# Optimization experiments

Hardware: AMD Instinct MI355X
Metric: run time of the kernel (lower is better)

The kernel has to match this reference:

```python
import jax, jax.numpy as jnp
import numpy as np

N = 50000
NEG_SLOPE = 0.2

def gat_conv(x, src, dst, W, a_src, a_dst, bias, heads, out_ch):
    # Linear projection per head: [N, H, C]
    h = (x @ W).reshape(x.shape[0], heads, out_ch)
    # Node-level attention terms alpha_src/alpha_dst: [N, H]
    al_src = jnp.einsum('nhc,hc->nh', h, a_src)
    al_dst = jnp.einsum('nhc,hc->nh', h, a_dst)
    # Edge logits with LeakyReLU: [E, H]
    logits = jax.nn.leaky_relu(al_src[src] + al_dst[dst], NEG_SLOPE)
    # Segment softmax over incoming edges of each dst node
    m = jax.ops.segment_max(logits, dst, num_segments=N)
    e = jnp.exp(logits - m[dst])
    s = jax.ops.segment_sum(e, dst, num_segments=N)
    alpha = e / (s[dst] + 1e-16)                      # [E, H]
    # Weighted message aggregation (scatter-add): [N, H, C]
    out = jax.ops.segment_sum(h[src] * alpha[..., None], dst, num_segments=N)
    return out.reshape(N, heads * out_ch) + bias


def setup_inputs() -> dict:
    key = jax.random.key(0)
    ks = jax.random.split(key, 12)
    in_ch, out_ch = 128, 256
    h1, c1 = 4, out_ch // 8          # conv1: 4 heads x 32
    mid = h1 * c1                    # 128 = out_ch // 2
    E = 1600000
    x = jax.random.normal(ks[0], (N, in_ch), jnp.float32)
    edge_index = jax.random.randint(ks[1], (2, E), 0, N, jnp.int64)
    sc = 0.1
    return {
        'x': x,
        'edge_index': edge_index,
        'W1': jax.random.normal(ks[2], (in_ch, h1 * c1), jnp.float32) * sc,
        'a_src1': jax.random.normal(ks[3], (h1, c1), jnp.float32) * sc,
        'a_dst1': jax.random.normal(ks[4], (h1, c1), jnp.float32) * sc,
        'b1': jnp.zeros((h1 * c1,), jnp.float32),
        'W2': jax.random.normal(ks[5], (mid, out_ch), jnp.float32) * sc,
        'a_src2': jax.random.normal(ks[6], (1, out_ch), jnp.float32) * sc,
        'a_dst2': jax.random.normal(ks[7], (1, out_ch), jnp.float32) * sc,
        'b2': jnp.zeros((out_ch,), jnp.float32),
    }


def reference(x, edge_index, W1, a_src1, a_dst1, b1, W2, a_src2, a_dst2, b2):
    # PyG GATConv adds self-loops by default
    loop = jnp.arange(N, dtype=edge_index.dtype)
    src = jnp.concatenate([edge_index[0], loop])
    dst = jnp.concatenate([edge_index[1], loop])
    h = gat_conv(x, src, dst, W1, a_src1, a_dst1, b1, heads=4, out_ch=32)
    h = jax.nn.relu(h)
    out = gat_conv(h, src, dst, W2, a_src2, a_dst2, b2, heads=1, out_ch=256)
    return out
```

## Files before the change

### kernel.cpp

```cpp
#include <hip/hip_runtime.h>
#include <hip/hip_fp16.h>
#include <math.h>

#define NSLOPE 0.2f

typedef _Float16 half8 __attribute__((ext_vector_type(8)));
typedef float floatx4 __attribute__((ext_vector_type(4)));

__device__ __forceinline__ float lrelu(float t) { return t > 0.f ? t : NSLOPE * t; }

__device__ __forceinline__ void fma8h(float* acc, float w, const uint4& v) {
    const __half2* h2 = reinterpret_cast<const __half2*>(&v);
#pragma unroll
    for (int i = 0; i < 4; ++i) {
        float2 f = __half22float2(h2[i]);
        acc[2 * i]     = fmaf(w, f.x, acc[2 * i]);
        acc[2 * i + 1] = fmaf(w, f.y, acc[2 * i + 1]);
    }
}

#define MAXB 5632
#define BE   8192

__global__ __launch_bounds__(256)
void prep_kernel(const int* __restrict__ dst, int* __restrict__ bcnt,
                 const float* __restrict__ x, __half* __restrict__ x16, int nx,
                 const float* __restrict__ W1, __half* __restrict__ W1T,
                 const float* __restrict__ W2, __half* __restrict__ W2T,
                 const float* __restrict__ a_src2, const float* __restrict__ a_dst2,
                 float* __restrict__ w2s, float* __restrict__ w2d,
                 int E, int Etot, int nb, int nbA, int ncast, int nt1, int nt2)
{
    __shared__ int hist[512];
    int bid = blockIdx.x;
    int tid = threadIdx.x;

    if (bid < nbA) {
        for (int i = tid; i < 512; i += 256) hist[i] = 0;
        __syncthreads();
        for (int e = bid * 256 + tid; e < Etot; e += nbA * 256) {
            int d = (e < E) ? dst[e] : (e - E);
            atomicAdd(&hist[d >> 7], 1);
        }
        __syncthreads();
        for (int i = tid; i < nb; i += 256) {
            int v = hist[i];
            if (v) atomicAdd(&bcnt[i], v);
        }
        return;
    }
    bid -= nbA;
    if (bid < ncast) {
        int i = (bid * 256 + tid) * 4;
        if (i < nx) {
            float4 v = *(const float4*)&x[i];
            __half2 a = __floats2half2_rn(v.x, v.y);
            __half2 b = __floats2half2_rn(v.z, v.w);
            *(uint2*)&x16[i] = make_uint2(*(unsigned*)&a, *(unsigned*)&b);
        }
        return;
    }
    bid -= ncast;
    if (bid < nt1) {
        int idx = bid * 256 + tid;
        int c = idx >> 7, k = idx & 127;
        W1T[(size_t)c * 128 + k] = __float2half(W1[(size_t)k * 128 + c]);
        return;
    }
    bid -= nt1;
    if (bid < nt2) {
        int idx = bid * 256 + tid;
        int c = idx >> 7, k = idx & 127;
        W2T[(size_t)c * 128 + k] = __float2half(W2[(size_t)k * 256 + c]);
        return;
    }
    {
        const float* a = (tid < 128) ? a_src2 : a_dst2;
        int k = tid & 127;
        float acc = 0.f;
        for (int c = 0; c < 256; c += 4) {
            float4 w = *(const float4*)&W2[(size_t)k * 256 + c];
            float4 av = *(const float4*)&a[c];
            acc = fmaf(w.x, av.x, fmaf(w.y, av.y, fmaf(w.z, av.z, fmaf(w.w, av.w, acc))));
        }
        if (tid < 128) w2s[k] = acc; else w2d[k] = acc;
    }
}

__global__ __launch_bounds__(512)
void scanBuckets_kernel(const int* __restrict__ bcnt, int* __restrict__ bbase,
                        int* __restrict__ gcur, int nb, int* __restrict__ offs,
                        int N, int total)
{
    __shared__ int tmp[512];
    int tid = threadIdx.x;
    int v = (tid < nb) ? bcnt[tid] : 0;
    tmp[tid] = v;
    __syncthreads();
    for (int off = 1; off < 512; off <<= 1) {
        int t = (tid >= off) ? tmp[tid - off] : 0;
        __syncthreads();
        tmp[tid] += t;
        __syncthreads();
    }
    if (tid < nb) {
        int e = tmp[tid] - v;
        bbase[tid] = e;
        gcur[tid] = e;
    }
    if (tid == 0) offs[N] = total;
}

__global__ __launch_bounds__(256)
void bucketB_kernel(const int* __restrict__ src, const int* __restrict__ dst,
                    int* __restrict__ gcur, unsigned* __restrict__ eout,
                    int E, int Etot, int nb)
{
    __shared__ int hist[512];
    __shared__ int res[512];
    __shared__ int lcur[512];
    int tid = threadIdx.x;
    int e0 = blockIdx.x * BE;
    int e1 = min(e0 + BE, Etot);

    for (int i = tid; i < 512; i += 256) hist[i] = 0;
    __syncthreads();
    for (int e = e0 + tid; e < e1; e += 256) {
        int d = (e < E) ? dst[e] : (e - E);
        atomicAdd(&hist[d >> 7], 1);
    }
    __syncthreads();
    for (int i = tid; i < nb; i += 256) {
        int h = hist[i];
        res[i] = h ? atomicAdd(&gcur[i], h) : 0;
        lcur[i] = 0;
    }
    __syncthreads();
    for (int e = e0 + tid; e < e1; e += 256) {
        int s, d;
        if (e < E) { s = src[e]; d = dst[e]; }
        else       { s = e - E; d = s; }
        int b = d >> 7;
        int p = res[b] + atomicAdd(&lcur[b], 1);
        eout[p] = (unsigned)s | ((unsigned)(d & 127) << 16);
    }
}

__global__ __launch_bounds__(256)
void combo_kernel(const unsigned* __restrict__ eout, const int* __restrict__ bbase,
                  const int* __restrict__ bcnt, unsigned short* __restrict__ csr,
                  int* __restrict__ offs, int N, int nb,
                  const __half* __restrict__ A16, const __half* __restrict__ W1T,
                  const float* __restrict__ a_src, const float* __restrict__ a_dst,
                  __half* __restrict__ h1, float* __restrict__ al_src,
                  float* __restrict__ al_dst)
{
    __shared__ unsigned eb[MAXB];
    __shared__ unsigned short sbuf[MAXB];
    __shared__ int cnt128[128], cur128[128], sc[128];

    int tid = threadIdx.x;
    if ((int)blockIdx.x < nb) {
        int b = blockIdx.x;
        int ebase = bbase[b];
        int ecnt = bcnt[b];
        int n0 = b << 7;
        int ncount = min(128, N - n0);

        if (tid < 128) cnt128[tid] = 0;
        for (int i = tid; i < ecnt; i += 256) eb[i] = eout[ebase + i];
        __syncthreads();
        for (int i = tid; i < ecnt; i += 256) atomicAdd(&cnt128[eb[i] >> 16], 1);
        __syncthreads();
        if (tid < 128) sc[tid] = cnt128[tid];
        __syncthreads();
        for (int off = 1; off < 128; off <<= 1) {
            int t = (tid >= off && tid < 128) ? sc[tid - off] : 0;
            __syncthreads();
            if (tid < 128) sc[tid] += t;
            __syncthreads();
        }
        if (tid < 128) {
            int excl = sc[tid] - cnt128[tid];
            cur128[tid] = excl;
            if (tid < ncount) offs[n0 + tid] = ebase + excl;
        }
        __syncthreads();
        for (int i = tid; i < ecnt; i += 256) {
            unsigned v = eb[i];
            int p = atomicAdd(&cur128[v >> 16], 1);
            sbuf[p] = (unsigned short)(v & 0xFFFFu);
        }
        __syncthreads();
        for (int i = tid; i < ecnt; i += 256) csr[ebase + i] = sbuf[i];
        return;
    }

    int gb = blockIdx.x - nb;
    int M = N;
    int wave = tid >> 6, lane = tid & 63;
    int lr = lane & 15, q = lane >> 4;
    int r0 = gb * 32 + (wave >> 1) * 16;
    int wcol = (wave & 1) * 64;

    int arow = min(r0 + lr, M - 1);
    const uint4* Arow = (const uint4*)A16 + (size_t)arow * 16;
    half8 a[4];
#pragma unroll
    for (int kb = 0; kb < 4; ++kb) {
        union { uint4 u; half8 h; } c;
        c.u = Arow[kb * 4 + q];
        a[kb] = c.h;
    }

    floatx4 acc[4];
    const floatx4 zero = {0.f, 0.f, 0.f, 0.f};
#pragma unroll
    for (int ct = 0; ct < 4; ++ct) acc[ct] = zero;

#pragma unroll
    for (int ct = 0; ct < 4; ++ct) {
        const uint4* Brow = (const uint4*)W1T + (size_t)(wcol + ct * 16 + lr) * 16;
#pragma unroll
        for (int kb = 0; kb < 4; ++kb) {
            union { uint4 u; half8 h; } c;
            c.u = Brow[kb * 4 + q];
            acc[ct] = __builtin_amdgcn_mfma_f32_16x16x32_f16(a[kb], c.h, acc[ct], 0, 0, 0);
        }
    }

#pragma unroll
    for (int ct = 0; ct < 4; ++ct) {
        int col = wcol + ct * 16 + lr;
#pragma unroll
        for (int r = 0; r < 4; ++r) {
            int row = r0 + q * 4 + r;
            if (row < M) h1[(size_t)row * 128 + col] = __float2half(acc[ct][r]);
        }
    }

    float as[4], ad[4];
#pragma unroll
    for (int ct = 0; ct < 4; ++ct) {
        int col = wcol + ct * 16 + lr;
        as[ct] = a_src[col];
        ad[ct] = a_dst[col];
    }
    int hb = wcol >> 5;
#pragma unroll
    for (int r = 0; r < 4; ++r) {
        float psA = acc[0][r] * as[0] + acc[1][r] * as[1];
        float psB = acc[2][r] * as[2] + acc[3][r] * as[3];
        float pdA = acc[0][r] * ad[0] + acc[1][r] * ad[1];
        float pdB = acc[2][r] * ad[2] + acc[3][r] * ad[3];
#pragma unroll
        for (int off = 1; off < 16; off <<= 1) {
            psA += __shfl_xor(psA, off); psB += __shfl_xor(psB, off);
            pdA += __shfl_xor(pdA, off); pdB += __shfl_xor(pdB, off);
        }
        if (lr == 0) {
            int row = r0 + q * 4 + r;
            if (row < M) {
                al_src[(size_t)row * 4 + hb]     = psA;
                al_src[(size_t)row * 4 + hb + 1] = psB;
                al_dst[(size_t)row * 4 + hb]     = pdA;
                al_dst[(size_t)row * 4 + hb + 1] = pdB;
            }
        }
    }
}

__global__ __launch_bounds__(256)
void gemm2_mfma(const __half* __restrict__ A16, const __half* __restrict__ W2T,
                const float* __restrict__ bias, float* __restrict__ out, int M)
{
    int wave = threadIdx.x >> 6, lane = threadIdx.x & 63;
    int lr = lane & 15, q = lane >> 4;
    int r0 = blockIdx.x * 16;
    int c0 = wave * 64;

    int arow = min(r0 + lr, M - 1);
    const uint4* Arow = (const uint4*)A16 + (size_t)arow * 16;
    half8 a[4];
#pragma unroll
    for (int kb = 0; kb < 4; ++kb) {
        union { uint4 u; half8 h; } c;
        c.u = Arow[kb * 4 + q];
        a[kb] = c.h;
    }

    floatx4 acc[4];
    const floatx4 zero = {0.f, 0.f, 0.f, 0.f};
#pragma unroll
    for (int ct = 0; ct < 4; ++ct) acc[ct] = zero;

#pragma unroll
    for (int ct = 0; ct < 4; ++ct) {
        const uint4* Brow = (const uint4*)W2T + (size_t)(c0 + ct * 16 + lr) * 16;
#pragma unroll
        for (int kb = 0; kb < 4; ++kb) {
            union { uint4 u; half8 h; } c;
            c.u = Brow[kb * 4 + q];
            acc[ct] = __builtin_amdgcn_mfma_f32_16x16x32_f16(a[kb], c.h, acc[ct], 0, 0, 0);
        }
    }

#pragma unroll
    for (int ct = 0; ct < 4; ++ct) {
        int col = c0 + ct * 16 + lr;
        float b = bias[col];
#pragma unroll
        for (int r = 0; r < 4; ++r) {
            int row = r0 + q * 4 + r;
            if (row < M) out[(size_t)row * 256 + col] = acc[ct][r] + b;
        }
    }
}

__global__ __launch_bounds__(256)
void agg1_kernel(const __half* __restrict__ feat, const unsigned short* __restrict__ csr_src,
                 const int* __restrict__ offs, const float* __restrict__ alS,
                 const float* __restrict__ alD, const float* __restrict__ bias,
                 const float* __restrict__ w2s, const float* __restrict__ w2d,
                 __half* __restrict__ hmid, float* __restrict__ alS2,
                 float* __restrict__ alD2, int N)
{
    int lane = threadIdx.x & 63;
    int n = blockIdx.x * 4 + (threadIdx.x >> 6);
    if (n >= N) return;

    int lc = lane & 15;
    int es = lane >> 4;
    int h = lc >> 2;

    float aD = alD[(size_t)n * 4 + h];
    int beg = offs[n], end = offs[n + 1];

    float acc0[8] = {0,0,0,0,0,0,0,0}, acc1[8] = {0,0,0,0,0,0,0,0};
    float sw0 = 0.f, sw1 = 0.f;
    const char* fbase = (const char*)feat + lc * 16;

    int j = beg + es;
    for (; j + 4 < end; j += 8) {
        int s0 = csr_src[j];
        int s1 = csr_src[j + 4];
        float w0 = __expf(lrelu(alS[(size_t)s0 * 4 + h] + aD));
        float w1 = __expf(lrelu(alS[(size_t)s1 * 4 + h] + aD));
        uint4 f0 = *(const uint4*)(fbase + (size_t)s0 * 256);
        uint4 f1 = *(const uint4*)(fbase + (size_t)s1 * 256);
        fma8h(acc0, w0, f0); sw0 += w0;
        fma8h(acc1, w1, f1); sw1 += w1;
    }
    if (j < end) {
        int s0 = csr_src[j];
        float w0 = __expf(lrelu(alS[(size_t)s0 * 4 + h] + aD));
        uint4 f0 = *(const uint4*)(fbase + (size_t)s0 * 256);
        fma8h(acc0, w0, f0); sw0 += w0;
    }

    float sw = sw0 + sw1;
    sw += __shfl_xor(sw, 16); sw += __shfl_xor(sw, 32);
#pragma unroll
    for (int i = 0; i < 8; ++i) {
        acc0[i] += acc1[i];
        acc0[i] += __shfl_xor(acc0[i], 16);
        acc0[i] += __shfl_xor(acc0[i], 32);
    }

    if (lane < 16) {
        float inv = 1.f / (sw + 1e-16f);
        float v[8];
#pragma unroll
        for (int i = 0; i < 8; ++i)
            v[i] = fmaxf(fmaf(acc0[i], inv, bias[lc * 8 + i]), 0.f);
        __half2 p0 = __floats2half2_rn(v[0], v[1]);
        __half2 p1 = __floats2half2_rn(v[2], v[3]);
        __half2 p2 = __floats2half2_rn(v[4], v[5]);
        __half2 p3 = __floats2half2_rn(v[6], v[7]);
        uint4 pk = make_uint4(*(unsigned*)&p0, *(unsigned*)&p1,
                              *(unsigned*)&p2, *(unsigned*)&p3);
        ((uint4*)hmid)[(size_t)n * 16 + lc] = pk;
        float ps = 0.f, pd = 0.f;
#pragma unroll
        for (int i = 0; i < 8; ++i) {
            ps = fmaf(v[i], w2s[lc * 8 + i], ps);
            pd = fmaf(v[i], w2d[lc * 8 + i], pd);
        }
        ps += __shfl_xor(ps, 1); ps += __shfl_xor(ps, 2);
        ps += __shfl_xor(ps, 4); ps += __shfl_xor(ps, 8);
        pd += __shfl_xor(pd, 1); pd += __shfl_xor(pd, 2);
        pd += __shfl_xor(pd, 4); pd += __shfl_xor(pd, 8);
        if (lane == 0) { alS2[n] = ps; alD2[n] = pd; }
    }
}

__global__ __launch_bounds__(256)
void agg2_kernel(const __half* __restrict__ feat, const unsigned short* __restrict__ csr_src,
                 const int* __restrict__ offs, const float* __restrict__ alS,
                 const float* __restrict__ alD, __half* __restrict__ m16, int N)
{
    int lane = threadIdx.x & 63;
    int n = blockIdx.x * 4 + (threadIdx.x >> 6);
    if (n >= N) return;

    int lc = lane & 15;
    int es = lane >> 4;

    float aD = alD[n];
    int beg = offs[n], end = offs[n + 1];

    float acc0[8] = {0,0,0,0,0,0,0,0}, acc1[8] = {0,0,0,0,0,0,0,0};
    float sw0 = 0.f, sw1 = 0.f;
    const char* fbase = (const char*)feat + lc * 16;

    int j = beg + es;
    for (; j + 4 < end; j += 8) {
        int s0 = csr_src[j];
        int s1 = csr_src[j + 4];
        float w0 = __expf(lrelu(alS[s0] + aD));
        float w1 = __expf(lrelu(alS[s1] + aD));
        uint4 f0 = *(const uint4*)(fbase + (size_t)s0 * 256);
        uint4 f1 = *(const uint4*)(fbase + (size_t)s1 * 256);
        fma8h(acc0, w0, f0); sw0 += w0;
        fma8h(acc1, w1, f1); sw1 += w1;
    }
    if (j < end) {
        int s0 = csr_src[j];
        float w0 = __expf(lrelu(alS[s0] + aD));
        uint4 f0 = *(const uint4*)(fbase + (size_t)s0 * 256);
        fma8h(acc0, w0, f0); sw0 += w0;
    }

    float sw = sw0 + sw1;
    sw += __shfl_xor(sw, 16); sw += __shfl_xor(sw, 32);
#pragma unroll
    for (int i = 0; i < 8; ++i) {
        acc0[i] += acc1[i];
        acc0[i] += __shfl_xor(acc0[i], 16);
        acc0[i] += __shfl_xor(acc0[i], 32);
    }

    if (lane < 16) {
        float inv = 1.f / (sw + 1e-16f);
        float v[8];
#pragma unroll
        for (int i = 0; i < 8; ++i) v[i] = acc0[i] * inv;
        __half2 p0 = __floats2half2_rn(v[0], v[1]);
        __half2 p1 = __floats2half2_rn(v[2], v[3]);
        __half2 p2 = __floats2half2_rn(v[4], v[5]);
        __half2 p3 = __floats2half2_rn(v[6], v[7]);
        uint4 pk = make_uint4(*(unsigned*)&p0, *(unsigned*)&p1,
                              *(unsigned*)&p2, *(unsigned*)&p3);
        ((uint4*)m16)[(size_t)n * 16 + lc] = pk;
    }
}

extern "C" void kernel_launch(void* const* d_in, const int* in_sizes, int n_in,
                              void* d_out, int out_size, void* d_ws, size_t ws_size,
                              hipStream_t stream)
{
    const float* x      = (const float*)d_in[0];
    const int*   ei     = (const int*)d_in[1];
    const float* W1     = (const float*)d_in[2];
    const float* a_src1 = (const float*)d_in[3];
    const float* a_dst1 = (const float*)d_in[4];
    const float* b1     = (const float*)d_in[5];
    const float* W2     = (const float*)d_in[6];
    const float* a_src2 = (const float*)d_in[7];
    const float* a_dst2 = (const float*)d_in[8];
    const float* b2     = (const float*)d_in[9];

    const int N    = in_sizes[0] / 128;
    const int E    = in_sizes[1] / 2;
    const int Etot = E + N;
    const int* src = ei;
    const int* dst = ei + E;
    const int nb   = (N + 127) >> 7;

    char* ws = (char*)d_ws;
    size_t off = 0;
    auto carve = [&](size_t bytes) -> void* {
        void* p = ws + off;
        off += (bytes + 255) & ~(size_t)255;
        return p;
    };
    __half*  x16  = (__half*)carve((size_t)N * 128 * 2);
    __half*  h1   = (__half*)carve((size_t)N * 128 * 2);
    __half*  hmid = (__half*)carve((size_t)N * 128 * 2);
    __half*  m16  = (__half*)carve((size_t)N * 128 * 2);
    __half*  W1T  = (__half*)carve(128 * 128 * 2);
    __half*  W2T  = (__half*)carve(256 * 128 * 2);
    float*   alS1 = (float*)carve((size_t)N * 4 * 4);
    float*   alD1 = (float*)carve((size_t)N * 4 * 4);
    float*   alS2 = (float*)carve((size_t)N * 4);
    float*   alD2 = (float*)carve((size_t)N * 4);
    float*   w2s  = (float*)carve(128 * 4);
    float*   w2d  = (float*)carve(128 * 4);
    int*     offs = (int*)carve((size_t)(N + 1) * 4);
    int*     bcnt = (int*)carve(512 * 4);
    int*     bbas = (int*)carve(512 * 4);
    int*     gcur = (int*)carve(512 * 4);
    unsigned* eout = (unsigned*)carve((size_t)Etot * 4);
    unsigned short* csr = (unsigned short*)carve((size_t)Etot * 2);
    (void)ws_size; (void)n_in; (void)out_size;

    const int TB = 256;
    const int agrid = (N + 3) / 4;
    const int g1grid = (N + 31) / 32;
    const int g2grid = (N + 15) / 16;
    const int nx = N * 128;

    const int nbA   = 512;
    const int ncast = (nx / 4 + TB - 1) / TB;
    const int nt1   = (128 * 128 + TB - 1) / TB;
    const int nt2   = (256 * 128 + TB - 1) / TB;
    const int nprep = nbA + ncast + nt1 + nt2 + 1;

    hipMemsetAsync(bcnt, 0, 512 * 4, stream);

    prep_kernel<<<nprep, TB, 0, stream>>>(dst, bcnt, x, x16, nx, W1, W1T, W2, W2T,
                                          a_src2, a_dst2, w2s, w2d,
                                          E, Etot, nb, nbA, ncast, nt1, nt2);
    scanBuckets_kernel<<<1, 512, 0, stream>>>(bcnt, bbas, gcur, nb, offs, N, Etot);
    bucketB_kernel<<<(Etot + BE - 1) / BE, TB, 0, stream>>>(src, dst, gcur, eout, E, Etot, nb);
    combo_kernel<<<nb + g1grid, TB, 0, stream>>>(eout, bbas, bcnt, csr, offs, N, nb,
                                                 x16, W1T, a_src1, a_dst1, h1, alS1, alD1);
    agg1_kernel<<<agrid, TB, 0, stream>>>(h1, csr, offs, alS1, alD1, b1,
                                          w2s, w2d, hmid, alS2, alD2, N);
    agg2_kernel<<<agrid, TB, 0, stream>>>(hmid, csr, offs, alS2, alD2, m16, N);
    gemm2_mfma<<<g2grid, TB, 0, stream>>>(m16, W2T, b2, (float*)d_out, N);
}
```

Before: 317.1 us.

## Fold log2e into attention terms, use fma_mix and deeper edge unrolling

```diff
diff --git a/kernel.cpp b/kernel.cpp
--- a/kernel.cpp
+++ b/kernel.cpp
@@ -3,19 +3,26 @@
 #include <math.h>
 
 #define NSLOPE 0.2f
+#define LOG2E  1.44269504f
 
 typedef _Float16 half8 __attribute__((ext_vector_type(8)));
 typedef float floatx4 __attribute__((ext_vector_type(4)));
 
-__device__ __forceinline__ float lrelu(float t) { return t > 0.f ? t : NSLOPE * t; }
-
-__device__ __forceinline__ void fma8h(float* acc, float w, const uint4& v) {
-    const __half2* h2 = reinterpret_cast<const __half2*>(&v);
+__device__ __forceinline__ float wcalc(float t) {
+    float l = fmaxf(t, NSLOPE * t);
+    float r;
+    asm("v_exp_f32 %0, %1" : "=v"(r) : "v"(l));
+    return r;
+}
+
+__device__ __forceinline__ void fma_mix8(float* acc, float w, const uint4& v) {
+    const unsigned* u = reinterpret_cast<const unsigned*>(&v);
 #pragma unroll
     for (int i = 0; i < 4; ++i) {
-        float2 f = __half22float2(h2[i]);
-        acc[2 * i]     = fmaf(w, f.x, acc[2 * i]);
-        acc[2 * i + 1] = fmaf(w, f.y, acc[2 * i + 1]);
+        asm("v_fma_mix_f32 %0, %1, %2, %0 op_sel:[0,0,0] op_sel_hi:[1,0,0]"
+            : "+v"(acc[2 * i]) : "v"(u[i]), "v"(w));
+        asm("v_fma_mix_f32 %0, %1, %2, %0 op_sel:[1,0,0] op_sel_hi:[1,0,0]"
+            : "+v"(acc[2 * i + 1]) : "v"(u[i]), "v"(w));
     }
 }
 
@@ -83,7 +90,7 @@
             float4 av = *(const float4*)&a[c];
             acc = fmaf(w.x, av.x, fmaf(w.y, av.y, fmaf(w.z, av.z, fmaf(w.w, av.w, acc))));
         }
-        if (tid < 128) w2s[k] = acc; else w2d[k] = acc;
+        if (tid < 128) w2s[k] = acc * LOG2E; else w2d[k] = acc * LOG2E;
     }
 }
 
@@ -243,8 +250,8 @@
 #pragma unroll
     for (int ct = 0; ct < 4; ++ct) {
         int col = wcol + ct * 16 + lr;
-        as[ct] = a_src[col];
-        ad[ct] = a_dst[col];
+        as[ct] = a_src[col] * LOG2E;
+        ad[ct] = a_dst[col] * LOG2E;
     }
     int hb = wcol >> 5;
 #pragma unroll
@@ -339,23 +346,32 @@
     float acc0[8] = {0,0,0,0,0,0,0,0}, acc1[8] = {0,0,0,0,0,0,0,0};
     float sw0 = 0.f, sw1 = 0.f;
     const char* fbase = (const char*)feat + lc * 16;
+    const float* alSh = alS + h;
 
     int j = beg + es;
-    for (; j + 4 < end; j += 8) {
+    for (; j + 12 < end; j += 16) {
         int s0 = csr_src[j];
         int s1 = csr_src[j + 4];
-        float w0 = __expf(lrelu(alS[(size_t)s0 * 4 + h] + aD));
-        float w1 = __expf(lrelu(alS[(size_t)s1 * 4 + h] + aD));
+        int s2 = csr_src[j + 8];
+        int s3 = csr_src[j + 12];
+        float w0 = wcalc(alSh[(size_t)s0 * 4] + aD);
+        float w1 = wcalc(alSh[(size_t)s1 * 4] + aD);
+        float w2 = wcalc(alSh[(size_t)s2 * 4] + aD);
+        float w3 = wcalc(alSh[(size_t)s3 * 4] + aD);
         uint4 f0 = *(const uint4*)(fbase + (size_t)s0 * 256);
         uint4 f1 = *(const uint4*)(fbase + (size_t)s1 * 256);
-        fma8h(acc0, w0, f0); sw0 += w0;
-        fma8h(acc1, w1, f1); sw1 += w1;
-    }
-    if (j < end) {
+        uint4 f2 = *(const uint4*)(fbase + (size_t)s2 * 256);
+        uint4 f3 = *(const uint4*)(fbase + (size_t)s3 * 256);
+        fma_mix8(acc0, w0, f0); sw0 += w0;
+        fma_mix8(acc1, w1, f1); sw1 += w1;
+        fma_mix8(acc0, w2, f2); sw0 += w2;
+        fma_mix8(acc1, w3, f3); sw1 += w3;
+    }
+    for (; j < end; j += 4) {
         int s0 = csr_src[j];
-        float w0 = __expf(lrelu(alS[(size_t)s0 * 4 + h] + aD));
+        float w0 = wcalc(alSh[(size_t)s0 * 4] + aD);
         uint4 f0 = *(const uint4*)(fbase + (size_t)s0 * 256);
-        fma8h(acc0, w0, f0); sw0 += w0;
+        fma_mix8(acc0, w0, f0); sw0 += w0;
     }
 
     float sw = sw0 + sw1;
@@ -414,21 +430,29 @@
     const char* fbase = (const char*)feat + lc * 16;
 
     int j = beg + es;
-    for (; j + 4 < end; j += 8) {
+    for (; j + 12 < end; j += 16) {
         int s0 = csr_src[j];
         int s1 = csr_src[j + 4];
-        float w0 = __expf(lrelu(alS[s0] + aD));
-        float w1 = __expf(lrelu(alS[s1] + aD));
+        int s2 = csr_src[j + 8];
+        int s3 = csr_src[j + 12];
+        float w0 = wcalc(alS[s0] + aD);
+        float w1 = wcalc(alS[s1] + aD);
+        float w2 = wcalc(alS[s2] + aD);
+        float w3 = wcalc(alS[s3] + aD);
         uint4 f0 = *(const uint4*)(fbase + (size_t)s0 * 256);
         uint4 f1 = *(const uint4*)(fbase + (size_t)s1 * 256);
-        fma8h(acc0, w0, f0); sw0 += w0;
-        fma8h(acc1, w1, f1); sw1 += w1;
-    }
-    if (j < end) {
+        uint4 f2 = *(const uint4*)(fbase + (size_t)s2 * 256);
+        uint4 f3 = *(const uint4*)(fbase + (size_t)s3 * 256);
+        fma_mix8(acc0, w0, f0); sw0 += w0;
+        fma_mix8(acc1, w1, f1); sw1 += w1;
+        fma_mix8(acc0, w2, f2); sw0 += w2;
+        fma_mix8(acc1, w3, f3); sw1 += w3;
+    }
+    for (; j < end; j += 4) {
         int s0 = csr_src[j];
-        float w0 = __expf(lrelu(alS[s0] + aD));
+        float w0 = wcalc(alS[s0] + aD);
         uint4 f0 = *(const uint4*)(fbase + (size_t)s0 * 256);
-        fma8h(acc0, w0, f0); sw0 += w0;
+        fma_mix8(acc0, w0, f0); sw0 += w0;
     }
 
     float sw = sw0 + sw1;
```

After: 310.1 us. -2.2%, faster.
